# Kernel tuning notes

Measured on AMD Instinct MI355X. Metric: run time of the kernel, lower is better.

## Reference

```python
import jax, jax.numpy as jnp
import numpy as np

B, S, H = 2, 2048, 2048
NH, NKV, HD = 16, 4, 128
ROPE_BASE = 10000.0


def hbit_linear(x, w):
    # BitNet: 8-bit per-token absmax activation quant, ternary (2-bit) weight quant
    s = 127.0 / jnp.clip(jnp.max(jnp.abs(x), axis=-1, keepdims=True), 1e-5, None)
    xq = jnp.clip(jnp.round(x * s), -128, 127) / s
    ws = 1.0 / jnp.clip(jnp.mean(jnp.abs(w)), 1e-5, None)
    wq = jnp.clip(jnp.round(w * ws), -1, 1) / ws
    return xq @ wq.T


def rotate_half(x):
    h = x.shape[-1] // 2
    return jnp.concatenate([-x[..., h:], x[..., :h]], axis=-1)


def rope_cos_sin(position_ids, head_dim, dtype):
    inv_freq = 1.0 / (ROPE_BASE ** (jnp.arange(0, head_dim, 2, dtype=jnp.float32) / head_dim))
    freqs = position_ids.astype(jnp.float32)[..., None] * inv_freq[None, None, :]  # (b,s,hd/2)
    emb = jnp.concatenate([freqs, freqs], axis=-1)  # (b,s,hd)
    return jnp.cos(emb).astype(dtype)[:, :, None, :], jnp.sin(emb).astype(dtype)[:, :, None, :]


def setup_inputs() -> dict:
    key = jax.random.key(0)
    ks = jax.random.split(key, 5)
    xavier = lambda k, shp: jax.random.uniform(k, shp, jnp.float32, -1.0, 1.0) * np.sqrt(6.0 / (shp[0] + shp[1]))
    causal = jnp.where(jnp.tril(jnp.ones((S, S), bool)), 0.0, -1e9).astype(jnp.float32)[None, None]
    return {
        "hidden_states": jax.random.normal(ks[0], (B, S, H), jnp.float32),
        "attention_mask": causal,
        "Wq": xavier(ks[1], (H, H)),
        "Wk": xavier(ks[2], (NKV * HD, H)),
        "Wv": xavier(ks[3], (NKV * HD, H)),
        "Wo": xavier(ks[4], (H, H)),
        "position_ids": jnp.arange(S, dtype=jnp.int64 if jax.config.jax_enable_x64 else jnp.int32)[None, :],
    }


def reference(hidden_states, attention_mask, Wq, Wk, Wv, Wo, position_ids):
    b, s, _ = hidden_states.shape
    q = hbit_linear(hidden_states, Wq).reshape(b, s, NH, HD)
    k = hbit_linear(hidden_states, Wk).reshape(b, s, NKV, HD)
    v = hbit_linear(hidden_states, Wv).reshape(b, s, NKV, HD)
    cos, sin = rope_cos_sin(position_ids, HD, q.dtype)  # (1,s,1,hd)
    q = q * cos + rotate_half(q) * sin
    k = k * cos + rotate_half(k) * sin
    n_rep = NH // NKV
    k = jnp.repeat(k, n_rep, axis=2)  # (b,s,NH,hd)
    v = jnp.repeat(v, n_rep, axis=2)
    scale = 1.0 / np.sqrt(HD)
    scores = jnp.einsum("bqhd,bkhd->bhqk", q, k) * scale + attention_mask
    probs = jax.nn.softmax(scores, axis=-1)  # dropout inactive (eval)
    out = jnp.einsum("bhqk,bkhd->bqhd", probs, v).reshape(b, s, NH * HD)
    return hbit_linear(out, Wo)
```

## Files before the change

kernel.cpp:

```cpp
#include <hip/hip_runtime.h>
#include <hip/hip_bf16.h>

#define B_ 2
#define S_ 2048
#define H_ 2048
#define NH_ 16
#define NKV_ 4
#define HD_ 128
#define M_ (B_*S_)
#define KVD_ (NKV_*HD_)

typedef signed char s8;
typedef __attribute__((ext_vector_type(8))) short short8;
typedef __attribute__((ext_vector_type(4))) float f32x4;
typedef __attribute__((ext_vector_type(4))) int int4v;

__device__ __forceinline__ float loadf(const void* p, long i, int isb){
  if (isb) return __bfloat162float(((const __hip_bfloat16*)p)[i]);
  return ((const float*)p)[i];
}

__device__ __forceinline__ unsigned short f2bf(float f){
  union { float f; unsigned u; } v; v.f = f;
  unsigned r = v.u + 0x7FFF + ((v.u >> 16) & 1);
  return (unsigned short)(r >> 16);
}

__device__ __forceinline__ float bf2f(unsigned short b){
  union { unsigned u; float f; } v; v.u = ((unsigned)b) << 16; return v.f;
}

__device__ __forceinline__ void gl2lds16(const void* g, void* l){
  __builtin_amdgcn_global_load_lds(
      (const __attribute__((address_space(1))) void*)g,
      (__attribute__((address_space(3))) void*)l, 16, 0, 0);
}

__device__ __forceinline__ int detect_isb(const unsigned int* x){
  __shared__ int dsh[4];
  int t = threadIdx.x, cnt = 0;
  #pragma unroll
  for (int i = 0; i < 8; i++){
    unsigned e = (x[t + i*256] >> 7) & 0xFF;
    cnt += (e >= 90 && e <= 150) ? 1 : 0;
  }
  #pragma unroll
  for (int k = 32; k > 0; k >>= 1) cnt += __shfl_down(cnt, k, 64);
  if ((t & 63) == 0) dsh[t >> 6] = cnt;
  __syncthreads();
  return (dsh[0] + dsh[1] + dsh[2] + dsh[3]) > 1228;
}

__global__ void k_prep_aq(const void* x,
                          const void* Wq, const void* Wk, const void* Wv, const void* Wo,
                          float* wsum, float* ct, float* st,
                          float* srow, s8* xq){
  __shared__ float sh[256];
  int isb = detect_isb((const unsigned int*)x);
  int bid = blockIdx.x, t = threadIdx.x;
  if (bid < 2048){
    if (t < 64){
      float inv = exp2f(-(float)t * 0.20762050593045952f);
      float a = (float)bid * inv;
      float sn, cs; sincosf(a, &sn, &cs);
      ct[bid*64 + t] = cs; st[bid*64 + t] = sn;
    }
    const void* w; long n; int wi; long b0; int nb;
    if (bid < 768)       { w = Wq; wi = 0; n = (long)H_*H_;   b0 = bid;      nb = 768; }
    else if (bid < 1024) { w = Wk; wi = 1; n = (long)KVD_*H_; b0 = bid-768;  nb = 256; }
    else if (bid < 1280) { w = Wv; wi = 2; n = (long)KVD_*H_; b0 = bid-1024; nb = 256; }
    else                 { w = Wo; wi = 3; n = (long)H_*H_;   b0 = bid-1280; nb = 768; }
    float s = 0.f;
    for (long i = b0*256 + t; i < n; i += (long)nb*256) s += fabsf(loadf(w, i, isb));
    sh[t] = s; __syncthreads();
    for (int k = 128; k > 0; k >>= 1){ if (t < k) sh[t] += sh[t+k]; __syncthreads(); }
    if (t == 0) atomicAdd(&wsum[wi], sh[0]);
  } else {
    int r = bid - 2048;
    long base = (long)r * H_;
    float v[8];
    if (isb){
      uint4 wv = ((const uint4*)((const unsigned short*)x + base))[t];
      unsigned u[4] = {wv.x, wv.y, wv.z, wv.w};
      #pragma unroll
      for (int i = 0; i < 4; i++){
        v[2*i]   = bf2f((unsigned short)(u[i] & 0xFFFF));
        v[2*i+1] = bf2f((unsigned short)(u[i] >> 16));
      }
    } else {
      const float4* p = (const float4*)((const float*)x + base);
      float4 a = p[t*2], b2 = p[t*2+1];
      v[0]=a.x; v[1]=a.y; v[2]=a.z; v[3]=a.w; v[4]=b2.x; v[5]=b2.y; v[6]=b2.z; v[7]=b2.w;
    }
    float mx = 0.f;
    #pragma unroll
    for (int i = 0; i < 8; i++) mx = fmaxf(mx, fabsf(v[i]));
    sh[t] = mx; __syncthreads();
    for (int k = 128; k > 0; k >>= 1){ if (t < k) sh[t] = fmaxf(sh[t], sh[t+k]); __syncthreads(); }
    float s = 127.0f / fmaxf(sh[0], 1e-5f);
    if (t == 0) srow[r] = s;
    unsigned long long pk = 0;
    #pragma unroll
    for (int i = 0; i < 8; i++){
      float q = fminf(fmaxf(rintf(v[i] * s), -128.f), 127.f);
      pk |= ((unsigned long long)(unsigned char)(s8)q) << (8*i);
    }
    *(unsigned long long*)(xq + base + t*8) = pk;
  }
}

__global__ void k_wquant_all(const void* Wq, const void* Wk, const void* Wv, const void* Wo,
                             const void* x, const float* wsum,
                             s8* oq, s8* ok, s8* ov, s8* oo){
  int isb = detect_isb((const unsigned int*)x);
  int bid = blockIdx.x, t = threadIdx.x;
  const float cntq = (float)((long)H_*H_), cntkv = (float)((long)KVD_*H_);
  const void* w; s8* out; long n; int wi; long b0; int nb; float cnt;
  if (bid < 1024)      { w = Wq; out = oq; wi = 0; n = (long)H_*H_;   b0 = bid;       nb = 1024; cnt = cntq; }
  else if (bid < 1280) { w = Wk; out = ok; wi = 1; n = (long)KVD_*H_; b0 = bid-1024;  nb = 256;  cnt = cntkv; }
  else if (bid < 1536) { w = Wv; out = ov; wi = 2; n = (long)KVD_*H_; b0 = bid-1280;  nb = 256;  cnt = cntkv; }
  else                 { w = Wo; out = oo; wi = 3; n = (long)H_*H_;   b0 = bid-1536;  nb = 1024; cnt = cntq; }
  float mean = fmaxf(wsum[wi] / cnt, 1e-5f);
  float sc = 1.0f / mean;
  for (long i = b0*256 + t; i < n; i += (long)nb*256){
    float v = rintf(loadf(w, i, isb) * sc);
    v = fminf(fmaxf(v, -1.f), 1.f);
    out[i] = (s8)v;
  }
}

__global__ void k_aquant_bf16(const unsigned short* __restrict__ x, float* __restrict__ srow, s8* __restrict__ xq){
  __shared__ float sh[256];
  int r = blockIdx.x, t = threadIdx.x;
  long base = (long)r * H_;
  uint4 wv = ((const uint4*)(x + base))[t];
  unsigned u[4] = {wv.x, wv.y, wv.z, wv.w};
  float v[8];
  #pragma unroll
  for (int i = 0; i < 4; i++){
    v[2*i]   = bf2f((unsigned short)(u[i] & 0xFFFF));
    v[2*i+1] = bf2f((unsigned short)(u[i] >> 16));
  }
  float mx = 0.f;
  #pragma unroll
  for (int i = 0; i < 8; i++) mx = fmaxf(mx, fabsf(v[i]));
  sh[t] = mx; __syncthreads();
  for (int k = 128; k > 0; k >>= 1){ if (t < k) sh[t] = fmaxf(sh[t], sh[t+k]); __syncthreads(); }
  float s = 127.0f / fmaxf(sh[0], 1e-5f);
  if (t == 0) srow[r] = s;
  unsigned long long pk = 0;
  #pragma unroll
  for (int i = 0; i < 8; i++){
    float q = fminf(fmaxf(rintf(v[i] * s), -128.f), 127.f);
    pk |= ((unsigned long long)(unsigned char)(s8)q) << (8*i);
  }
  *(unsigned long long*)(xq + base + t*8) = pk;
}

__device__ __forceinline__ void gemm_core(
      const s8* __restrict__ A, const s8* __restrict__ Bw, s8* As, s8* Bs,
      const float* __restrict__ srow, float mean,
      void* __restrict__ Cout, int N, int mode, int isb,
      unsigned short* __restrict__ Vt,
      const float* __restrict__ ct, const float* __restrict__ st,
      long bcol, long arow){
  int tid = threadIdx.x;
  int wave = tid >> 6, lane = tid & 63;
  int quad = lane >> 4, c = lane & 15;
  int wm = wave >> 1, wn = wave & 1;
  const int K = H_;

  int4v acc[4][4];
  #pragma unroll
  for (int mt = 0; mt < 4; mt++)
    #pragma unroll
    for (int nt = 0; nt < 4; nt++) acc[mt][nt] = (int4v){0,0,0,0};

  int rl = lane >> 2;
  int kq = (lane & 3) ^ ((lane >> 3) & 3);
  int ch0 = wave*2, ch1 = wave*2 + 1;
  long gA0 = (arow + ch0*16 + rl)*(long)K + kq*16;
  long gA1 = (arow + ch1*16 + rl)*(long)K + kq*16;
  long gB0 = (bcol + ch0*16 + rl)*(long)K + kq*16;
  long gB1 = (bcol + ch1*16 + rl)*(long)K + kq*16;

  int sA = quad ^ ((c >> 1) & 3);
  int ntl[4];
  #pragma unroll
  for (int nt = 0; nt < 4; nt++) ntl[nt] = 2*wn + (nt & 1) + 4*(nt >> 1);
  int frA[4], frB[4];
  #pragma unroll
  for (int mt = 0; mt < 4; mt++) frA[mt] = (wm*64 + mt*16 + c)*64 + sA*16;
  #pragma unroll
  for (int nt = 0; nt < 4; nt++) frB[nt] = (ntl[nt]*16 + c)*64 + sA*16;

  for (int k0 = 0; k0 < K; k0 += 128){
    gl2lds16(A  + gA0 + k0,      As        + ch0*1024);
    gl2lds16(A  + gA1 + k0,      As        + ch1*1024);
    gl2lds16(Bw + gB0 + k0,      Bs        + ch0*1024);
    gl2lds16(Bw + gB1 + k0,      Bs        + ch1*1024);
    gl2lds16(A  + gA0 + k0 + 64, As + 8192 + ch0*1024);
    gl2lds16(A  + gA1 + k0 + 64, As + 8192 + ch1*1024);
    gl2lds16(Bw + gB0 + k0 + 64, Bs + 8192 + ch0*1024);
    gl2lds16(Bw + gB1 + k0 + 64, Bs + 8192 + ch1*1024);
    __syncthreads();
    #pragma unroll
    for (int s = 0; s < 2; s++){
      const s8* Ab = As + s*8192;
      const s8* Bb = Bs + s*8192;
      int4v afr[4], bfr[4];
      #pragma unroll
      for (int mt = 0; mt < 4; mt++) afr[mt] = *(const int4v*)&Ab[frA[mt]];
      #pragma unroll
      for (int nt = 0; nt < 4; nt++) bfr[nt] = *(const int4v*)&Bb[frB[nt]];
      #pragma unroll
      for (int mt = 0; mt < 4; mt++)
        #pragma unroll
        for (int nt = 0; nt < 4; nt++)
          acc[mt][nt] = __builtin_amdgcn_mfma_i32_16x16x64_i8(afr[mt], bfr[nt], acc[mt][nt], 0, 0, 0);
    }
    __syncthreads();
  }

  if (mode == 0 || mode == 3){
    unsigned short* Ob = (unsigned short*)Cout;
    #pragma unroll
    for (int mt = 0; mt < 4; mt++){
      #pragma unroll
      for (int r = 0; r < 4; r++){
        long grow = arow + wm*64 + mt*16 + quad*4 + r;
        float sc = mean / srow[grow];
        if (mode == 0) sc *= 0.12751743f;
        int pos = (int)(grow & (S_-1));
        #pragma unroll
        for (int p = 0; p < 2; p++){
          int col_lo = (int)bcol + (2*wn + p)*16 + c;
          int d = col_lo & 63;
          float cv = ct[pos*64 + d], sv = st[pos*64 + d];
          float vlo = acc[mt][p][r]   * sc;
          float vhi = acc[mt][p+2][r] * sc;
          Ob[grow*(long)N + col_lo]      = f2bf(vlo*cv - vhi*sv);
          Ob[grow*(long)N + col_lo + 64] = f2bf(vhi*cv + vlo*sv);
        }
      }
    }
  } else if (mode == 1){
    #pragma unroll
    for (int mt = 0; mt < 4; mt++){
      long grow0 = arow + wm*64 + mt*16 + quad*4;
      float s0 = mean / srow[grow0];
      float s1 = mean / srow[grow0+1];
      float s2 = mean / srow[grow0+2];
      float s3 = mean / srow[grow0+3];
      long bb = grow0 >> 11; int sI = (int)(grow0 & (S_-1));
      unsigned short* base = Vt + bb*(long)KVD_*S_ + sI;
      #pragma unroll
      for (int nt = 0; nt < 4; nt++){
        float v0 = acc[mt][nt][0]*s0, v1 = acc[mt][nt][1]*s1;
        float v2 = acc[mt][nt][2]*s2, v3 = acc[mt][nt][3]*s3;
        unsigned lo, hi;
        asm("v_cvt_pk_bf16_f32 %0, %1, %2" : "=v"(lo) : "v"(v0), "v"(v1));
        asm("v_cvt_pk_bf16_f32 %0, %1, %2" : "=v"(hi) : "v"(v2), "v"(v3));
        uint2 pk; pk.x = lo; pk.y = hi;
        *(uint2*)(base + (long)(bcol + ntl[nt]*16 + c)*S_) = pk;
      }
    }
  } else {
    #pragma unroll
    for (int mt = 0; mt < 4; mt++){
      #pragma unroll
      for (int r = 0; r < 4; r++){
        long grow = arow + wm*64 + mt*16 + quad*4 + r;
        float sc = mean / srow[grow];
        long cb = grow*(long)N + bcol + c;
        if (isb){
          __hip_bfloat16* o = (__hip_bfloat16*)Cout;
          #pragma unroll
          for (int nt = 0; nt < 4; nt++)
            o[cb + ntl[nt]*16] = __float2bfloat16(acc[mt][nt][r] * sc);
        } else {
          float* o = (float*)Cout;
          #pragma unroll
          for (int nt = 0; nt < 4; nt++)
            o[cb + ntl[nt]*16] = acc[mt][nt][r] * sc;
        }
      }
    }
  }
}

__global__ __launch_bounds__(256, 2) void k_gemm_qkv(
      const s8* __restrict__ xq,
      const s8* __restrict__ wqq, const s8* __restrict__ wkq, const s8* __restrict__ wvq,
      const float* __restrict__ srow, const float* __restrict__ wsum,
      unsigned short* __restrict__ Qb, unsigned short* __restrict__ Kb,
      unsigned short* __restrict__ Vt,
      const float* __restrict__ ct, const float* __restrict__ st){
  __shared__ __align__(16) s8 As[2*128*64];
  __shared__ __align__(16) s8 Bs[2*128*64];
  int lid = blockIdx.x;
  int xcd = lid & 7;
  int rem = lid >> 3;
  int by  = xcd*4 + (rem & 3);
  int bx  = rem >> 2;
  const float cntq = (float)((long)H_*H_), cntkv = (float)((long)KVD_*H_);
  const s8* Bw; void* Cout; unsigned short* vt = nullptr;
  int N, mode; float mean; long bcol;
  if (bx < 16){
    Bw = wqq; Cout = Qb; N = H_;   mode = 0; mean = fmaxf(wsum[0]/cntq, 1e-5f);  bcol = (long)bx*128;
  } else if (bx < 20){
    Bw = wkq; Cout = Kb; N = KVD_; mode = 3; mean = fmaxf(wsum[1]/cntkv, 1e-5f); bcol = (long)(bx-16)*128;
  } else {
    Bw = wvq; Cout = nullptr; vt = Vt; N = KVD_; mode = 1; mean = fmaxf(wsum[2]/cntkv, 1e-5f); bcol = (long)(bx-20)*128;
  }
  gemm_core(xq, Bw, As, Bs, srow, mean, Cout, N, mode, 0, vt, ct, st, bcol, (long)by*128);
}

__global__ __launch_bounds__(256, 2) void k_gemm_o(
      const s8* __restrict__ aq, const s8* __restrict__ woq,
      const float* __restrict__ srow, const float* __restrict__ wsum,
      const void* __restrict__ x, void* __restrict__ out,
      const float* __restrict__ ct, const float* __restrict__ st){
  __shared__ __align__(16) s8 As[2*128*64];
  __shared__ __align__(16) s8 Bs[2*128*64];
  int isb = detect_isb((const unsigned int*)x);
  int lid = blockIdx.x;
  int xcd = lid & 7;
  int rem = lid >> 3;
  int by  = xcd*4 + (rem & 3);
  int bx  = rem >> 2;
  float mean = fmaxf(wsum[3] / (float)((long)H_*H_), 1e-5f);
  gemm_core(aq, woq, As, Bs, srow, mean, out, H_, 2, isb, nullptr, ct, st,
            (long)bx*128, (long)by*128);
}

#define PSTR 40
__global__ __launch_bounds__(256) void k_attn_mfma(const unsigned short* __restrict__ Qb,
    const unsigned short* __restrict__ Kb, const unsigned short* __restrict__ Vt,
    unsigned short* __restrict__ ob){
  int wid = threadIdx.x >> 6, lane = threadIdx.x & 63;
  int quad = lane >> 4, c = lane & 15;
  int kvh = blockIdx.y, b = blockIdx.z;
  int win = blockIdx.x;
  if (b == 1) win = (S_/32 - 1) - win;
  int h = kvh*4 + wid;
  int q0 = win*32;

  __shared__ __align__(16) unsigned short Ks[2][64*128];
  __shared__ __align__(16) unsigned short Vs[128*64];
  __shared__ __align__(16) unsigned short Ps[4][16*PSTR];

  short8 qf[2][4];
  #pragma unroll
  for (int t0 = 0; t0 < 2; t0++)
    #pragma unroll
    for (int f = 0; f < 4; f++)
      qf[t0][f] = *(const short8*)(Qb + ((long)(b*S_ + q0 + t0*16 + c)*NH_ + h)*HD_ + f*32 + quad*8);

  const unsigned short* Kg = Kb + (long)b*S_*KVD_ + kvh*HD_;
  const unsigned short* Vg = Vt + ((long)b*KVD_ + kvh*HD_)*S_;

  f32x4 o[2][8], ol[2];
  #pragma unroll
  for (int t0 = 0; t0 < 2; t0++){
    #pragma unroll
    for (int i = 0; i < 8; i++) o[t0][i] = (f32x4){0.f,0.f,0.f,0.f};
    ol[t0] = (f32x4){0.f,0.f,0.f,0.f};
  }
  short8 ones;
  #pragma unroll
  for (int i = 0; i < 8; i++) ones[i] = (short)0x3F80;

  int skey = lane >> 4;
  int kslot = lane & 15;
  int vrow = lane >> 3;
  int vslot = lane & 7;

  int nk = q0 + 32;
  #pragma unroll
  for (int i = 0; i < 4; i++){
    int kk = wid*16 + i*4;
    int key = kk + skey;
    int g = kslot ^ (key & 15);
    gl2lds16(Kg + (long)key*KVD_ + g*8, &Ks[0][kk*128]);
  }

  int buf = 0;
  for (int kc = 0; kc < nk; kc += 64, buf ^= 1){
    __syncthreads();
    #pragma unroll
    for (int i = 0; i < 4; i++){
      int rr = wid*32 + i*8;
      int hd = rr + vrow;
      int g = vslot ^ (hd & 7);
      gl2lds16(Vg + (long)hd*S_ + kc + g*8, &Vs[rr*64]);
    }

    f32x4 s[2][4];
    #pragma unroll
    for (int t0 = 0; t0 < 2; t0++)
      #pragma unroll
      for (int kt = 0; kt < 4; kt++) s[t0][kt] = (f32x4){0.f,0.f,0.f,0.f};
    #pragma unroll
    for (int kt = 0; kt < 4; kt++){
      short8 kf4[4];
      #pragma unroll
      for (int f = 0; f < 4; f++)
        kf4[f] = *(const short8*)&Ks[buf][(kt*16 + c)*128 + ((f*4 + quad) ^ c)*8];
      #pragma unroll
      for (int t0 = 0; t0 < 2; t0++)
        #pragma unroll
        for (int f = 0; f < 4; f++)
          s[t0][kt] = __builtin_amdgcn_mfma_f32_16x16x32_bf16(kf4[f], qf[t0][f], s[t0][kt], 0, 0, 0);
    }
    #pragma unroll
    for (int t0 = 0; t0 < 2; t0++){
      int qv = q0 + t0*16 + c;
      if (kc + 63 > q0 + t0*16){
        #pragma unroll
        for (int kt = 0; kt < 4; kt++){
          #pragma unroll
          for (int r = 0; r < 4; r++){
            int key = kc + kt*16 + quad*4 + r;
            if (key > qv) s[t0][kt][r] = -1e30f;
          }
        }
      }
    }

    __syncthreads();

    if (kc + 64 < nk){
      #pragma unroll
      for (int i = 0; i < 4; i++){
        int kk = wid*16 + i*4;
        int key = kk + skey;
        int g = kslot ^ (key & 15);
        gl2lds16(Kg + (long)(kc + 64 + key)*KVD_ + g*8, &Ks[buf^1][kk*128]);
      }
    }

    #pragma unroll
    for (int pp = 0; pp < 2; pp++){
      short8 vf[8];
      #pragma unroll
      for (int nt = 0; nt < 8; nt++)
        vf[nt] = *(const short8*)&Vs[(nt*16 + c)*64 + ((pp*4 + quad) ^ (c & 7))*8];
      #pragma unroll
      for (int t0 = 0; t0 < 2; t0++){
        #pragma unroll
        for (int tk = 0; tk < 2; tk++){
          f32x4 sv = s[t0][pp*2 + tk];
          float e0 = exp2f(sv[0]), e1 = exp2f(sv[1]);
          float e2 = exp2f(sv[2]), e3 = exp2f(sv[3]);
          unsigned w0, w1;
          asm("v_cvt_pk_bf16_f32 %0, %1, %2" : "=v"(w0) : "v"(e0), "v"(e1));
          asm("v_cvt_pk_bf16_f32 %0, %1, %2" : "=v"(w1) : "v"(e2), "v"(e3));
          uint2 pkv; pkv.x = w0; pkv.y = w1;
          *(uint2*)&Ps[wid][c*PSTR + tk*16 + quad*4] = pkv;
        }
        short8 pf = *(const short8*)&Ps[wid][c*PSTR + quad*8];
        #pragma unroll
        for (int nt = 0; nt < 8; nt++)
          o[t0][nt] = __builtin_amdgcn_mfma_f32_16x16x32_bf16(pf, vf[nt], o[t0][nt], 0, 0, 0);
        ol[t0] = __builtin_amdgcn_mfma_f32_16x16x32_bf16(pf, ones, ol[t0], 0, 0, 0);
      }
    }
  }

  #pragma unroll
  for (int t0 = 0; t0 < 2; t0++){
    float il[4];
    #pragma unroll
    for (int r = 0; r < 4; r++) il[r] = 1.0f / ol[t0][r];
    #pragma unroll
    for (int nt = 0; nt < 8; nt++)
      #pragma unroll
      for (int r = 0; r < 4; r++)
        ob[((long)(b*S_ + q0 + t0*16 + quad*4 + r))*H_ + h*HD_ + nt*16 + c] = f2bf(o[t0][nt][r]*il[r]);
  }
}

extern "C" void kernel_launch(void* const* d_in, const int* in_sizes, int n_in,
                              void* d_out, int out_size, void* d_ws, size_t ws_size,
                              hipStream_t stream){
  (void)in_sizes; (void)n_in; (void)out_size; (void)ws_size;
  const void* x  = d_in[0];
  const void* Wq = d_in[2];
  const void* Wk = d_in[3];
  const void* Wv = d_in[4];
  const void* Wo = d_in[5];
  char* ws = (char*)d_ws;
  size_t o = 0;
  auto alloc = [&](size_t b){ size_t r = o; o += (b + 255) & ~(size_t)255; return r; };
  size_t META = alloc(256);
  float* wsum = (float*)(ws + META);
  float* s_x = (float*)(ws + alloc((size_t)M_*4));
  float* s_a = (float*)(ws + alloc((size_t)M_*4));
  float* ct  = (float*)(ws + alloc((size_t)S_*64*4));
  float* st  = (float*)(ws + alloc((size_t)S_*64*4));
  s8* xq  = (s8*)(ws + alloc((size_t)M_*H_));
  s8* wqq = (s8*)(ws + alloc((size_t)H_*H_));
  s8* wkq = (s8*)(ws + alloc((size_t)KVD_*H_));
  s8* wvq = (s8*)(ws + alloc((size_t)KVD_*H_));
  s8* woq = (s8*)(ws + alloc((size_t)H_*H_));
  unsigned short* Qb = (unsigned short*)(ws + alloc((size_t)M_*NH_*HD_*2));
  unsigned short* Kb = (unsigned short*)(ws + alloc((size_t)M_*KVD_*2));
  unsigned short* Vt = (unsigned short*)(ws + alloc((size_t)M_*KVD_*2));
  unsigned short* ab = (unsigned short*)(ws + alloc((size_t)M_*H_*2));
  s8* aq = xq;

  hipMemsetAsync(ws + META, 0, 64, stream);

  k_prep_aq<<<2048 + M_, 256, 0, stream>>>(x, Wq, Wk, Wv, Wo, wsum, ct, st, s_x, xq);

  k_wquant_all<<<2560, 256, 0, stream>>>(Wq, Wk, Wv, Wo, x, wsum, wqq, wkq, wvq, woq);

  k_gemm_qkv<<<768, 256, 0, stream>>>(xq, wqq, wkq, wvq, s_x, wsum, Qb, Kb, Vt, ct, st);

  dim3 ga(S_/32, NKV_, B_);
  k_attn_mfma<<<ga, 256, 0, stream>>>(Qb, Kb, Vt, ab);

  k_aquant_bf16<<<M_, 256, 0, stream>>>(ab, s_a, aq);

  k_gemm_o<<<512, 256, 0, stream>>>(aq, woq, s_a, wsum, x, d_out, ct, st);
}
```

Before: 289.7 us.

## Fuse all stages into one persistent megakernel with software grid barriers

Replaces the six kernel launches with a single persistent kernel of 768 blocks that runs each stage in turn (weight scan and activation quant, weight quant, QKV GEMM, attention, output activation quant, O GEMM), separated by atomic-counter grid barriers. The aim is to remove launch gaps and tail effects between stages. It falls back to the separate kernels if occupancy is below 3 blocks per CU or register use is too high. Risks include deadlock if not all blocks are co-resident, since the barrier has only a guard timeout. Attention also runs on 512 of the 768 blocks with shared memory sized for the largest stage, which can leave CUs idle and lower occupancy.

```diff
diff --git a/kernel.cpp b/kernel.cpp
--- a/kernel.cpp
+++ b/kernel.cpp
@@ -9,6 +9,8 @@
 #define HD_ 128
 #define M_ (B_*S_)
 #define KVD_ (NKV_*HD_)
+#define PSTR 40
+#define GRID_MEGA 768
 
 typedef signed char s8;
 typedef __attribute__((ext_vector_type(8))) short short8;
@@ -36,8 +38,22 @@
       (__attribute__((address_space(3))) void*)l, 16, 0, 0);
 }
 
-__device__ __forceinline__ int detect_isb(const unsigned int* x){
-  __shared__ int dsh[4];
+__device__ __forceinline__ void gridbar(unsigned* bar, unsigned target){
+  __syncthreads();
+  if (threadIdx.x == 0){
+    __threadfence();
+    atomicAdd(bar, 1u);
+    unsigned guard = 0;
+    while (atomicAdd(bar, 0u) < target){
+      __builtin_amdgcn_s_sleep(2);
+      if (++guard > (1u<<22)) break;
+    }
+    __threadfence();
+  }
+  __syncthreads();
+}
+
+__device__ __forceinline__ int detect_isb_s(const unsigned int* x, int* dsh){
   int t = threadIdx.x, cnt = 0;
   #pragma unroll
   for (int i = 0; i < 8; i++){
@@ -48,79 +64,25 @@
   for (int k = 32; k > 0; k >>= 1) cnt += __shfl_down(cnt, k, 64);
   if ((t & 63) == 0) dsh[t >> 6] = cnt;
   __syncthreads();
-  return (dsh[0] + dsh[1] + dsh[2] + dsh[3]) > 1228;
-}
-
-__global__ void k_prep_aq(const void* x,
-                          const void* Wq, const void* Wk, const void* Wv, const void* Wo,
-                          float* wsum, float* ct, float* st,
-                          float* srow, s8* xq){
-  __shared__ float sh[256];
-  int isb = detect_isb((const unsigned int*)x);
-  int bid = blockIdx.x, t = threadIdx.x;
-  if (bid < 2048){
-    if (t < 64){
-      float inv = exp2f(-(float)t * 0.20762050593045952f);
-      float a = (float)bid * inv;
-      float sn, cs; sincosf(a, &sn, &cs);
-      ct[bid*64 + t] = cs; st[bid*64 + t] = sn;
-    }
-    const void* w; long n; int wi; long b0; int nb;
-    if (bid < 768)       { w = Wq; wi = 0; n = (long)H_*H_;   b0 = bid;      nb = 768; }
-    else if (bid < 1024) { w = Wk; wi = 1; n = (long)KVD_*H_; b0 = bid-768;  nb = 256; }
-    else if (bid < 1280) { w = Wv; wi = 2; n = (long)KVD_*H_; b0 = bid-1024; nb = 256; }
-    else                 { w = Wo; wi = 3; n = (long)H_*H_;   b0 = bid-1280; nb = 768; }
-    float s = 0.f;
-    for (long i = b0*256 + t; i < n; i += (long)nb*256) s += fabsf(loadf(w, i, isb));
-    sh[t] = s; __syncthreads();
-    for (int k = 128; k > 0; k >>= 1){ if (t < k) sh[t] += sh[t+k]; __syncthreads(); }
-    if (t == 0) atomicAdd(&wsum[wi], sh[0]);
-  } else {
-    int r = bid - 2048;
-    long base = (long)r * H_;
-    float v[8];
-    if (isb){
-      uint4 wv = ((const uint4*)((const unsigned short*)x + base))[t];
-      unsigned u[4] = {wv.x, wv.y, wv.z, wv.w};
-      #pragma unroll
-      for (int i = 0; i < 4; i++){
-        v[2*i]   = bf2f((unsigned short)(u[i] & 0xFFFF));
-        v[2*i+1] = bf2f((unsigned short)(u[i] >> 16));
-      }
-    } else {
-      const float4* p = (const float4*)((const float*)x + base);
-      float4 a = p[t*2], b2 = p[t*2+1];
-      v[0]=a.x; v[1]=a.y; v[2]=a.z; v[3]=a.w; v[4]=b2.x; v[5]=b2.y; v[6]=b2.z; v[7]=b2.w;
-    }
-    float mx = 0.f;
-    #pragma unroll
-    for (int i = 0; i < 8; i++) mx = fmaxf(mx, fabsf(v[i]));
-    sh[t] = mx; __syncthreads();
-    for (int k = 128; k > 0; k >>= 1){ if (t < k) sh[t] = fmaxf(sh[t], sh[t+k]); __syncthreads(); }
-    float s = 127.0f / fmaxf(sh[0], 1e-5f);
-    if (t == 0) srow[r] = s;
-    unsigned long long pk = 0;
-    #pragma unroll
-    for (int i = 0; i < 8; i++){
-      float q = fminf(fmaxf(rintf(v[i] * s), -128.f), 127.f);
-      pk |= ((unsigned long long)(unsigned char)(s8)q) << (8*i);
-    }
-    *(unsigned long long*)(xq + base + t*8) = pk;
-  }
-}
-
-__global__ void k_wquant_all(const void* Wq, const void* Wk, const void* Wv, const void* Wo,
-                             const void* x, const float* wsum,
-                             s8* oq, s8* ok, s8* ov, s8* oo){
-  int isb = detect_isb((const unsigned int*)x);
-  int bid = blockIdx.x, t = threadIdx.x;
-  const float cntq = (float)((long)H_*H_), cntkv = (float)((long)KVD_*H_);
-  const void* w; s8* out; long n; int wi; long b0; int nb; float cnt;
-  if (bid < 1024)      { w = Wq; out = oq; wi = 0; n = (long)H_*H_;   b0 = bid;       nb = 1024; cnt = cntq; }
-  else if (bid < 1280) { w = Wk; out = ok; wi = 1; n = (long)KVD_*H_; b0 = bid-1024;  nb = 256;  cnt = cntkv; }
-  else if (bid < 1536) { w = Wv; out = ov; wi = 2; n = (long)KVD_*H_; b0 = bid-1280;  nb = 256;  cnt = cntkv; }
-  else                 { w = Wo; out = oo; wi = 3; n = (long)H_*H_;   b0 = bid-1536;  nb = 1024; cnt = cntq; }
-  float mean = fmaxf(wsum[wi] / cnt, 1e-5f);
+  int r = (dsh[0] + dsh[1] + dsh[2] + dsh[3]) > 1228;
+  __syncthreads();
+  return r;
+}
+
+__device__ __forceinline__ void wscan_seg(const void* w, long n, long b0, int nb,
+                                          int isb, float* wsum_i, float* sh){
+  int t = threadIdx.x;
+  float s = 0.f;
+  for (long i = b0*256 + t; i < n; i += (long)nb*256) s += fabsf(loadf(w, i, isb));
+  sh[t] = s; __syncthreads();
+  for (int k = 128; k > 0; k >>= 1){ if (t < k) sh[t] += sh[t+k]; __syncthreads(); }
+  if (t == 0) atomicAdd(wsum_i, sh[0]);
+  __syncthreads();
+}
+
+__device__ __forceinline__ void wquant_seg(const void* w, s8* out, long n, long b0, int nb,
+                                           float mean, int isb){
+  int t = threadIdx.x;
   float sc = 1.0f / mean;
   for (long i = b0*256 + t; i < n; i += (long)nb*256){
     float v = rintf(loadf(w, i, isb) * sc);
@@ -129,17 +91,23 @@
   }
 }
 
-__global__ void k_aquant_bf16(const unsigned short* __restrict__ x, float* __restrict__ srow, s8* __restrict__ xq){
-  __shared__ float sh[256];
-  int r = blockIdx.x, t = threadIdx.x;
-  long base = (long)r * H_;
-  uint4 wv = ((const uint4*)(x + base))[t];
-  unsigned u[4] = {wv.x, wv.y, wv.z, wv.w};
+__device__ __forceinline__ void aquant_row_x(const void* x, int isb, long r,
+                                             float* srow, s8* xq, float* sh){
+  int t = threadIdx.x;
+  long base = r * H_;
   float v[8];
-  #pragma unroll
-  for (int i = 0; i < 4; i++){
-    v[2*i]   = bf2f((unsigned short)(u[i] & 0xFFFF));
-    v[2*i+1] = bf2f((unsigned short)(u[i] >> 16));
+  if (isb){
+    uint4 wv = ((const uint4*)((const unsigned short*)x + base))[t];
+    unsigned u[4] = {wv.x, wv.y, wv.z, wv.w};
+    #pragma unroll
+    for (int i = 0; i < 4; i++){
+      v[2*i]   = bf2f((unsigned short)(u[i] & 0xFFFF));
+      v[2*i+1] = bf2f((unsigned short)(u[i] >> 16));
+    }
+  } else {
+    const float4* p = (const float4*)((const float*)x + base);
+    float4 a = p[t*2], b2 = p[t*2+1];
+    v[0]=a.x; v[1]=a.y; v[2]=a.z; v[3]=a.w; v[4]=b2.x; v[5]=b2.y; v[6]=b2.z; v[7]=b2.w;
   }
   float mx = 0.f;
   #pragma unroll
@@ -155,6 +123,36 @@
     pk |= ((unsigned long long)(unsigned char)(s8)q) << (8*i);
   }
   *(unsigned long long*)(xq + base + t*8) = pk;
+  __syncthreads();
+}
+
+__device__ __forceinline__ void aquant_row_ab(const unsigned short* x, long r,
+                                              float* srow, s8* xq, float* sh){
+  int t = threadIdx.x;
+  long base = r * H_;
+  uint4 wv = ((const uint4*)(x + base))[t];
+  unsigned u[4] = {wv.x, wv.y, wv.z, wv.w};
+  float v[8];
+  #pragma unroll
+  for (int i = 0; i < 4; i++){
+    v[2*i]   = bf2f((unsigned short)(u[i] & 0xFFFF));
+    v[2*i+1] = bf2f((unsigned short)(u[i] >> 16));
+  }
+  float mx = 0.f;
+  #pragma unroll
+  for (int i = 0; i < 8; i++) mx = fmaxf(mx, fabsf(v[i]));
+  sh[t] = mx; __syncthreads();
+  for (int k = 128; k > 0; k >>= 1){ if (t < k) sh[t] = fmaxf(sh[t], sh[t+k]); __syncthreads(); }
+  float s = 127.0f / fmaxf(sh[0], 1e-5f);
+  if (t == 0) srow[r] = s;
+  unsigned long long pk = 0;
+  #pragma unroll
+  for (int i = 0; i < 8; i++){
+    float q = fminf(fmaxf(rintf(v[i] * s), -128.f), 127.f);
+    pk |= ((unsigned long long)(unsigned char)(s8)q) << (8*i);
+  }
+  *(unsigned long long*)(xq + base + t*8) = pk;
+  __syncthreads();
 }
 
 __device__ __forceinline__ void gemm_core(
@@ -289,42 +287,31 @@
   }
 }
 
-__global__ __launch_bounds__(256, 2) void k_gemm_qkv(
-      const s8* __restrict__ xq,
-      const s8* __restrict__ wqq, const s8* __restrict__ wkq, const s8* __restrict__ wvq,
-      const float* __restrict__ srow, const float* __restrict__ wsum,
-      unsigned short* __restrict__ Qb, unsigned short* __restrict__ Kb,
-      unsigned short* __restrict__ Vt,
-      const float* __restrict__ ct, const float* __restrict__ st){
-  __shared__ __align__(16) s8 As[2*128*64];
-  __shared__ __align__(16) s8 Bs[2*128*64];
-  int lid = blockIdx.x;
+__device__ __forceinline__ void qkv_tile(int lid, const s8* xq,
+      const s8* wqq, const s8* wkq, const s8* wvq,
+      const float* srow, const float* wsum,
+      unsigned short* Qb, unsigned short* Kb, unsigned short* Vt,
+      const float* ct, const float* st, s8* As, s8* Bs){
   int xcd = lid & 7;
   int rem = lid >> 3;
   int by  = xcd*4 + (rem & 3);
   int bx  = rem >> 2;
-  const float cntq = (float)((long)H_*H_), cntkv = (float)((long)KVD_*H_);
+  const float cq = (float)((long)H_*H_), ck = (float)((long)KVD_*H_);
   const s8* Bw; void* Cout; unsigned short* vt = nullptr;
   int N, mode; float mean; long bcol;
   if (bx < 16){
-    Bw = wqq; Cout = Qb; N = H_;   mode = 0; mean = fmaxf(wsum[0]/cntq, 1e-5f);  bcol = (long)bx*128;
+    Bw = wqq; Cout = Qb; N = H_;   mode = 0; mean = fmaxf(wsum[0]/cq, 1e-5f);  bcol = (long)bx*128;
   } else if (bx < 20){
-    Bw = wkq; Cout = Kb; N = KVD_; mode = 3; mean = fmaxf(wsum[1]/cntkv, 1e-5f); bcol = (long)(bx-16)*128;
+    Bw = wkq; Cout = Kb; N = KVD_; mode = 3; mean = fmaxf(wsum[1]/ck, 1e-5f); bcol = (long)(bx-16)*128;
   } else {
-    Bw = wvq; Cout = nullptr; vt = Vt; N = KVD_; mode = 1; mean = fmaxf(wsum[2]/cntkv, 1e-5f); bcol = (long)(bx-20)*128;
+    Bw = wvq; Cout = nullptr; vt = Vt; N = KVD_; mode = 1; mean = fmaxf(wsum[2]/ck, 1e-5f); bcol = (long)(bx-20)*128;
   }
   gemm_core(xq, Bw, As, Bs, srow, mean, Cout, N, mode, 0, vt, ct, st, bcol, (long)by*128);
 }
 
-__global__ __launch_bounds__(256, 2) void k_gemm_o(
-      const s8* __restrict__ aq, const s8* __restrict__ woq,
-      const float* __restrict__ srow, const float* __restrict__ wsum,
-      const void* __restrict__ x, void* __restrict__ out,
-      const float* __restrict__ ct, const float* __restrict__ st){
-  __shared__ __align__(16) s8 As[2*128*64];
-  __shared__ __align__(16) s8 Bs[2*128*64];
-  int isb = detect_isb((const unsigned int*)x);
-  int lid = blockIdx.x;
+__device__ __forceinline__ void o_tile(int lid, const s8* aq, const s8* woq,
+      const float* srow, const float* wsum, int isb, void* out,
+      const float* ct, const float* st, s8* As, s8* Bs){
   int xcd = lid & 7;
   int rem = lid >> 3;
   int by  = xcd*4 + (rem & 3);
@@ -334,21 +321,15 @@
             (long)bx*128, (long)by*128);
 }
 
-#define PSTR 40
-__global__ __launch_bounds__(256) void k_attn_mfma(const unsigned short* __restrict__ Qb,
-    const unsigned short* __restrict__ Kb, const unsigned short* __restrict__ Vt,
-    unsigned short* __restrict__ ob){
+__device__ __forceinline__ void attn_body(int win, int kvh, int b,
+    const unsigned short* __restrict__ Qb, const unsigned short* __restrict__ Kb,
+    const unsigned short* __restrict__ Vt, unsigned short* __restrict__ ob,
+    unsigned short (*Ks)[64*128], unsigned short* Vs, unsigned short (*Ps)[16*PSTR]){
   int wid = threadIdx.x >> 6, lane = threadIdx.x & 63;
   int quad = lane >> 4, c = lane & 15;
-  int kvh = blockIdx.y, b = blockIdx.z;
-  int win = blockIdx.x;
   if (b == 1) win = (S_/32 - 1) - win;
   int h = kvh*4 + wid;
   int q0 = win*32;
-
-  __shared__ __align__(16) unsigned short Ks[2][64*128];
-  __shared__ __align__(16) unsigned short Vs[128*64];
-  __shared__ __align__(16) unsigned short Ps[4][16*PSTR];
 
   short8 qf[2][4];
   #pragma unroll
@@ -481,6 +462,145 @@
   }
 }
 
+
+__global__ void k_prep_aq(const void* x,
+                          const void* Wq, const void* Wk, const void* Wv, const void* Wo,
+                          float* wsum, float* ct, float* st,
+                          float* srow, s8* xq){
+  __shared__ __align__(16) float sh[256];
+  __shared__ int dsh[4];
+  int isb = detect_isb_s((const unsigned int*)x, dsh);
+  int bid = blockIdx.x, t = threadIdx.x;
+  if (bid < 2048){
+    if (t < 64){
+      float inv = exp2f(-(float)t * 0.20762050593045952f);
+      float a = (float)bid * inv;
+      float sn, cs; sincosf(a, &sn, &cs);
+      ct[bid*64 + t] = cs; st[bid*64 + t] = sn;
+    }
+    if (bid < 768)       wscan_seg(Wq, (long)H_*H_,   bid,      768, isb, &wsum[0], sh);
+    else if (bid < 1024) wscan_seg(Wk, (long)KVD_*H_, bid-768,  256, isb, &wsum[1], sh);
+    else if (bid < 1280) wscan_seg(Wv, (long)KVD_*H_, bid-1024, 256, isb, &wsum[2], sh);
+    else                 wscan_seg(Wo, (long)H_*H_,   bid-1280, 768, isb, &wsum[3], sh);
+  } else {
+    aquant_row_x(x, isb, bid - 2048, srow, xq, sh);
+  }
+}
+
+__global__ void k_wquant_all(const void* Wq, const void* Wk, const void* Wv, const void* Wo,
+                             const void* x, const float* wsum,
+                             s8* oq, s8* ok, s8* ov, s8* oo){
+  __shared__ int dsh[4];
+  int isb = detect_isb_s((const unsigned int*)x, dsh);
+  int bid = blockIdx.x;
+  const float cq = (float)((long)H_*H_), ck = (float)((long)KVD_*H_);
+  if (bid < 1024)      wquant_seg(Wq, oq, (long)H_*H_,   bid,      1024, fmaxf(wsum[0]/cq, 1e-5f), isb);
+  else if (bid < 1280) wquant_seg(Wk, ok, (long)KVD_*H_, bid-1024, 256,  fmaxf(wsum[1]/ck, 1e-5f), isb);
+  else if (bid < 1536) wquant_seg(Wv, ov, (long)KVD_*H_, bid-1280, 256,  fmaxf(wsum[2]/ck, 1e-5f), isb);
+  else                 wquant_seg(Wo, oo, (long)H_*H_,   bid-1536, 1024, fmaxf(wsum[3]/cq, 1e-5f), isb);
+}
+
+__global__ void k_aquant_bf16(const unsigned short* __restrict__ x,
+                              float* __restrict__ srow, s8* __restrict__ xq){
+  __shared__ __align__(16) float sh[256];
+  aquant_row_ab(x, blockIdx.x, srow, xq, sh);
+}
+
+__global__ __launch_bounds__(256, 2) void k_gemm_qkv(
+      const s8* __restrict__ xq,
+      const s8* __restrict__ wqq, const s8* __restrict__ wkq, const s8* __restrict__ wvq,
+      const float* __restrict__ srow, const float* __restrict__ wsum,
+      unsigned short* __restrict__ Qb, unsigned short* __restrict__ Kb,
+      unsigned short* __restrict__ Vt,
+      const float* __restrict__ ct, const float* __restrict__ st){
+  __shared__ __align__(16) s8 As[2*128*64];
+  __shared__ __align__(16) s8 Bs[2*128*64];
+  qkv_tile(blockIdx.x, xq, wqq, wkq, wvq, srow, wsum, Qb, Kb, Vt, ct, st, As, Bs);
+}
+
+__global__ __launch_bounds__(256, 2) void k_gemm_o(
+      const s8* __restrict__ aq, const s8* __restrict__ woq,
+      const float* __restrict__ srow, const float* __restrict__ wsum,
+      const void* __restrict__ x, void* __restrict__ out,
+      const float* __restrict__ ct, const float* __restrict__ st){
+  __shared__ __align__(16) s8 As[2*128*64];
+  __shared__ __align__(16) s8 Bs[2*128*64];
+  __shared__ int dsh[4];
+  int isb = detect_isb_s((const unsigned int*)x, dsh);
+  o_tile(blockIdx.x, aq, woq, srow, wsum, isb, out, ct, st, As, Bs);
+}
+
+__global__ __launch_bounds__(256) void k_attn_mfma(const unsigned short* __restrict__ Qb,
+    const unsigned short* __restrict__ Kb, const unsigned short* __restrict__ Vt,
+    unsigned short* __restrict__ ob){
+  __shared__ __align__(16) unsigned short Ks[2][64*128];
+  __shared__ __align__(16) unsigned short Vs[128*64];
+  __shared__ __align__(16) unsigned short Ps[4][16*PSTR];
+  attn_body(blockIdx.x, blockIdx.y, blockIdx.z, Qb, Kb, Vt, ob, Ks, Vs, Ps);
+}
+
+struct SmemAttn { unsigned short Ks[2][64*128]; unsigned short Vs[128*64]; unsigned short Ps[4][16*PSTR]; };
+struct SmemGemm { s8 As[2*128*64]; s8 Bs[2*128*64]; };
+
+__global__ __launch_bounds__(256, 3) void k_mega(
+    const void* x, const void* Wq, const void* Wk, const void* Wv, const void* Wo,
+    float* wsum, unsigned* bars, float* ct, float* st, float* s_x, s8* xq,
+    s8* wqq, s8* wkq, s8* wvq, s8* woq,
+    unsigned short* Qb, unsigned short* Kb, unsigned short* Vt,
+    unsigned short* ab, float* s_a, s8* aq, void* out){
+  __shared__ __align__(16) unsigned char smem[sizeof(SmemAttn)];
+  float* sh = (float*)smem;
+  int*  dsh = (int*)(smem + 1024);
+  int bid = blockIdx.x, t = threadIdx.x;
+  int isb = detect_isb_s((const unsigned int*)x, dsh);
+
+  {
+    long idx = (long)bid*256 + t;
+    if (idx < (long)S_*64){
+      int pos = (int)(idx >> 6), d = (int)(idx & 63);
+      float inv = exp2f(-(float)d * 0.20762050593045952f);
+      float a = (float)pos * inv;
+      float sn, cs; sincosf(a, &sn, &cs);
+      ct[pos*64 + d] = cs; st[pos*64 + d] = sn;
+    }
+    if (bid < 288)      wscan_seg(Wq, (long)H_*H_,   bid,     288, isb, &wsum[0], sh);
+    else if (bid < 384) wscan_seg(Wk, (long)KVD_*H_, bid-288, 96,  isb, &wsum[1], sh);
+    else if (bid < 480) wscan_seg(Wv, (long)KVD_*H_, bid-384, 96,  isb, &wsum[2], sh);
+    else                wscan_seg(Wo, (long)H_*H_,   bid-480, 288, isb, &wsum[3], sh);
+    for (long r = bid; r < M_; r += GRID_MEGA) aquant_row_x(x, isb, r, s_x, xq, sh);
+  }
+  gridbar(&bars[0], GRID_MEGA);
+
+  {
+    const float cq = (float)((long)H_*H_), ck = (float)((long)KVD_*H_);
+    if (bid < 288)      wquant_seg(Wq, wqq, (long)H_*H_,   bid,     288, fmaxf(wsum[0]/cq, 1e-5f), isb);
+    else if (bid < 384) wquant_seg(Wk, wkq, (long)KVD_*H_, bid-288, 96,  fmaxf(wsum[1]/ck, 1e-5f), isb);
+    else if (bid < 480) wquant_seg(Wv, wvq, (long)KVD_*H_, bid-384, 96,  fmaxf(wsum[2]/ck, 1e-5f), isb);
+    else                wquant_seg(Wo, woq, (long)H_*H_,   bid-480, 288, fmaxf(wsum[3]/cq, 1e-5f), isb);
+  }
+  gridbar(&bars[1], GRID_MEGA);
+
+  {
+    SmemGemm* sg = (SmemGemm*)smem;
+    qkv_tile(bid, xq, wqq, wkq, wvq, s_x, wsum, Qb, Kb, Vt, ct, st, sg->As, sg->Bs);
+  }
+  gridbar(&bars[2], GRID_MEGA);
+
+  if (bid < 512){
+    SmemAttn* sa = (SmemAttn*)smem;
+    attn_body(bid & 63, (bid >> 6) & 3, bid >> 8, Qb, Kb, Vt, ab, sa->Ks, sa->Vs, sa->Ps);
+  }
+  gridbar(&bars[3], GRID_MEGA);
+
+  for (long r = bid; r < M_; r += GRID_MEGA) aquant_row_ab(ab, r, s_a, aq, sh);
+  gridbar(&bars[4], GRID_MEGA);
+
+  if (bid < 512){
+    SmemGemm* sg = (SmemGemm*)smem;
+    o_tile(bid, aq, woq, s_a, wsum, isb, out, ct, st, sg->As, sg->Bs);
+  }
+}
+
 extern "C" void kernel_launch(void* const* d_in, const int* in_sizes, int n_in,
                               void* d_out, int out_size, void* d_ws, size_t ws_size,
                               hipStream_t stream){
@@ -495,6 +615,7 @@
   auto alloc = [&](size_t b){ size_t r = o; o += (b + 255) & ~(size_t)255; return r; };
   size_t META = alloc(256);
   float* wsum = (float*)(ws + META);
+  unsigned* bars = (unsigned*)(ws + META + 64);
   float* s_x = (float*)(ws + alloc((size_t)M_*4));
   float* s_a = (float*)(ws + alloc((size_t)M_*4));
   float* ct  = (float*)(ws + alloc((size_t)S_*64*4));
@@ -508,20 +629,33 @@
   unsigned short* Kb = (unsigned short*)(ws + alloc((size_t)M_*KVD_*2));
   unsigned short* Vt = (unsigned short*)(ws + alloc((size_t)M_*KVD_*2));
   unsigned short* ab = (unsigned short*)(ws + alloc((size_t)M_*H_*2));
-  s8* aq = xq;
-
-  hipMemsetAsync(ws + META, 0, 64, stream);
+  s8* aq = (s8*)(ws + alloc((size_t)M_*H_));
+  void* outp = d_out;
+
+  hipMemsetAsync(ws + META, 0, 256, stream);
+
+  static int mega_ok = -1;
+  if (mega_ok < 0){
+    hipFuncAttributes fa{};
+    int occ = 0;
+    hipError_t e1 = hipFuncGetAttributes(&fa, (const void*)k_mega);
+    hipError_t e2 = hipOccupancyMaxActiveBlocksPerMultiprocessor(&occ, (const void*)k_mega, 256, 0);
+    mega_ok = (e1 == hipSuccess && e2 == hipSuccess &&
+               occ >= 3 && fa.numRegs > 0 && fa.numRegs <= 168) ? 1 : 0;
+  }
+
+  if (mega_ok == 1){
+    k_mega<<<GRID_MEGA, 256, 0, stream>>>(
+        x, Wq, Wk, Wv, Wo, wsum, bars, ct, st, s_x, xq,
+        wqq, wkq, wvq, woq, Qb, Kb, Vt, ab, s_a, aq, outp);
+    return;
+  }
 
   k_prep_aq<<<2048 + M_, 256, 0, stream>>>(x, Wq, Wk, Wv, Wo, wsum, ct, st, s_x, xq);
-
   k_wquant_all<<<2560, 256, 0, stream>>>(Wq, Wk, Wv, Wo, x, wsum, wqq, wkq, wvq, woq);
-
   k_gemm_qkv<<<768, 256, 0, stream>>>(xq, wqq, wkq, wvq, s_x, wsum, Qb, Kb, Vt, ct, st);
-
   dim3 ga(S_/32, NKV_, B_);
   k_attn_mfma<<<ga, 256, 0, stream>>>(Qb, Kb, Vt, ab);
-
   k_aquant_bf16<<<M_, 256, 0, stream>>>(ab, s_a, aq);
-
   k_gemm_o<<<512, 256, 0, stream>>>(aq, woq, s_a, wsum, x, d_out, ct, st);
 }
```

Result: no change. 291.8 us (+0.7%).
